# Performance work log

Hardware: AMD Instinct MI355X
Metric: run time of the kernel (lower is better)

## Reference

```python
import jax, jax.numpy as jnp
import numpy as np

BN_EPS = 1e-5  # torch BatchNorm1d default


def setup_inputs() -> dict:
    key = jax.random.key(0)
    ks = jax.random.split(key, 4)
    S, B, H = 2048, 64, 1024
    return {
        "ctx": jax.random.normal(ks[0], (S, B, H), dtype=jnp.float32),
        "key": jax.random.normal(ks[1], (B, H), dtype=jnp.float32),
        "mask": jnp.zeros((B, S), dtype=jnp.float32),
        "fc1_w": jax.random.normal(ks[2], (H, 2 * H), dtype=jnp.float32) * 0.02,
        "fc1_b": jnp.zeros((H,), dtype=jnp.float32),
        "bn_gamma": jnp.ones((H,), dtype=jnp.float32),
        "bn_beta": jnp.zeros((H,), dtype=jnp.float32),
        "fc2_w": jax.random.normal(ks[3], (H, H), dtype=jnp.float32) * 0.02,
        "fc2_b": jnp.zeros((H,), dtype=jnp.float32),
    }


def reference(ctx, key, mask, fc1_w, fc1_b, bn_gamma, bn_beta, fc2_w, fc2_b):
    # ctx: (S, B, H) -> (B, S, H)
    ctx_b = jnp.transpose(ctx, (1, 0, 2))
    # dot-product scores: (B, S)
    At = jnp.einsum('bsh,bh->bs', ctx_b, key) + mask
    At = jax.nn.softmax(At, axis=1)
    # weighted sum of context: (B, H)
    attn = jnp.einsum('bs,bsh->bh', At, ctx_b)
    # MLP head: Linear -> BatchNorm1d (training stats, biased var) -> Tanh -> Linear
    x = jnp.concatenate([attn, key], axis=1)  # (B, 2H)
    x = x @ fc1_w.T + fc1_b
    mean = jnp.mean(x, axis=0)
    var = jnp.mean(jnp.square(x - mean), axis=0)
    x = (x - mean) * jax.lax.rsqrt(var + BN_EPS) * bn_gamma + bn_beta
    x = jnp.tanh(x)
    x = x @ fc2_w.T + fc2_b
    return (x, At)
```

## Files before the change

### kernel.cpp

```cpp
#include <hip/hip_runtime.h>

constexpr int Sdim = 2048;
constexpr int Bdim = 64;
constexpr int Hdim = 1024;
constexpr int NCHUNK = 16;
constexpr int KS1 = 16;
constexpr int KS2 = 8;

constexpr int PM_OFF   = 0;
constexpr int PL_OFF   = 1024;
constexpr int PACC_OFF = 2048;
constexpr int ATTN_OFF = PACC_OFF + Bdim * NCHUNK * Hdim;
constexpr int XMID_OFF = ATTN_OFF + Bdim * Hdim;
constexpr int P1_OFF   = XMID_OFF + Bdim * Hdim;
constexpr int P2_OFF   = P1_OFF + KS1 * Bdim * Hdim;

__global__ __launch_bounds__(256) void k1_attn(const float* __restrict__ ctx,
                                               const float* __restrict__ key,
                                               const float* __restrict__ mask,
                                               float* __restrict__ ws,
                                               float* __restrict__ At) {
    const int chunk = blockIdx.x;
    const int b     = blockIdx.y;
    const int t     = threadIdx.x;
    const int lane  = t & 63;
    const int wave  = t >> 6;

    const float4* key4 = (const float4*)(key + (size_t)b * Hdim);
    float4 kr[4];
#pragma unroll
    for (int j = 0; j < 4; ++j) kr[j] = key4[j * 64 + lane];

    float4 acc[4];
#pragma unroll
    for (int j = 0; j < 4; ++j) acc[j] = make_float4(0.f, 0.f, 0.f, 0.f);
    float m = -1e30f, l = 0.f;

    const int s0 = chunk * 128 + wave * 32;
    for (int i = 0; i < 32; ++i) {
        const int s = s0 + i;
        const float4* c4 = (const float4*)ctx + (((size_t)s * Bdim + b) << 8);
        float4 v[4];
#pragma unroll
        for (int j = 0; j < 4; ++j) v[j] = c4[j * 64 + lane];

        float d = 0.f;
#pragma unroll
        for (int j = 0; j < 4; ++j)
            d += v[j].x * kr[j].x + v[j].y * kr[j].y + v[j].z * kr[j].z + v[j].w * kr[j].w;
#pragma unroll
        for (int off = 32; off >= 1; off >>= 1) d += __shfl_xor(d, off, 64);
        d += mask[b * Sdim + s];
        if (lane == 0) At[b * Sdim + s] = d;

        const float nm = fmaxf(m, d);
        const float sc = __expf(m - nm);
        const float w  = __expf(d - nm);
#pragma unroll
        for (int j = 0; j < 4; ++j) {
            acc[j].x = acc[j].x * sc + v[j].x * w;
            acc[j].y = acc[j].y * sc + v[j].y * w;
            acc[j].z = acc[j].z * sc + v[j].z * w;
            acc[j].w = acc[j].w * sc + v[j].w * w;
        }
        l = l * sc + w;
        m = nm;
    }

    __shared__ float lm[4], ll[4];
    __shared__ __align__(16) float lacc[4][1024];
    if (lane == 0) { lm[wave] = m; ll[wave] = l; }
    __syncthreads();
    const float M  = fmaxf(fmaxf(lm[0], lm[1]), fmaxf(lm[2], lm[3]));
    const float scw = __expf(m - M);
    float4* lw = (float4*)lacc[wave];
#pragma unroll
    for (int j = 0; j < 4; ++j)
        lw[j * 64 + lane] = make_float4(acc[j].x * scw, acc[j].y * scw,
                                        acc[j].z * scw, acc[j].w * scw);
    __syncthreads();

    const float L = ll[0] * __expf(lm[0] - M) + ll[1] * __expf(lm[1] - M)
                  + ll[2] * __expf(lm[2] - M) + ll[3] * __expf(lm[3] - M);
    const float4* l4 = (const float4*)lacc;
    float4 r = l4[t];
#pragma unroll
    for (int wv = 1; wv < 4; ++wv) {
        float4 o = l4[wv * 256 + t];
        r.x += o.x; r.y += o.y; r.z += o.z; r.w += o.w;
    }
    ((float4*)(ws + PACC_OFF))[(b * NCHUNK + chunk) * 256 + t] = r;
    if (t == 0) {
        ws[PM_OFF + b * NCHUNK + chunk] = M;
        ws[PL_OFF + b * NCHUNK + chunk] = L;
    }
}

__global__ __launch_bounds__(256) void k2_final(float* __restrict__ ws,
                                                float* __restrict__ At) {
    const int b = blockIdx.x;
    const int t = threadIdx.x;

    float pm[NCHUNK];
    float M = -1e30f;
#pragma unroll
    for (int c = 0; c < NCHUNK; ++c) {
        pm[c] = ws[PM_OFF + b * NCHUNK + c];
        M = fmaxf(M, pm[c]);
    }
    float e[NCHUNK];
    float L = 0.f;
#pragma unroll
    for (int c = 0; c < NCHUNK; ++c) {
        e[c] = __expf(pm[c] - M);
        L += ws[PL_OFF + b * NCHUNK + c] * e[c];
    }
    const float invL = 1.f / L;

    const float4* pa = (const float4*)(ws + PACC_OFF);
    float4 r = make_float4(0.f, 0.f, 0.f, 0.f);
#pragma unroll
    for (int c = 0; c < NCHUNK; ++c) {
        float4 v = pa[(b * NCHUNK + c) * 256 + t];
        r.x += v.x * e[c]; r.y += v.y * e[c]; r.z += v.z * e[c]; r.w += v.w * e[c];
    }
    r.x *= invL; r.y *= invL; r.z *= invL; r.w *= invL;
    ((float4*)(ws + ATTN_OFF))[b * 256 + t] = r;

#pragma unroll
    for (int k = 0; k < Sdim / 256; ++k) {
        const int s = t + k * 256;
        At[b * Sdim + s] = __expf(At[b * Sdim + s] - M) * invL;
    }
}

__global__ __launch_bounds__(256) void k3a_fc1(const float* __restrict__ attn,
                                               const float* __restrict__ key,
                                               const float* __restrict__ w,
                                               float* __restrict__ part) {
    const int obase = blockIdx.x * 64;
    const int kblk  = blockIdx.y;
    const int t  = threadIdx.x;
    const int bx = (t & 15) * 4;
    const int ox = (t >> 4) * 4;

    __shared__ __align__(16) float xs[32][68];
    __shared__ __align__(16) float wsh[32][68];

    float a[4][4];
#pragma unroll
    for (int i = 0; i < 4; ++i)
#pragma unroll
        for (int j = 0; j < 4; ++j) a[i][j] = 0.f;

    for (int c = 0; c < 4; ++c) {
        const int i0 = kblk * 128 + c * 32;
        const float* src = (i0 < Hdim) ? (attn + i0) : (key + (i0 - Hdim));
#pragma unroll
        for (int j = 0; j < 8; ++j) {
            const int e = t + j * 256;
            const int k_l = e & 31, b_l = e >> 5;
            xs[k_l][b_l] = src[b_l * Hdim + k_l];
        }
#pragma unroll
        for (int j = 0; j < 8; ++j) {
            const int e = t + j * 256;
            const int k_l = e & 31, o_l = e >> 5;
            wsh[k_l][o_l] = w[(size_t)(obase + o_l) * 2048 + i0 + k_l];
        }
        __syncthreads();
#pragma unroll
        for (int k = 0; k < 32; ++k) {
            const float4 xv = *(const float4*)&xs[k][bx];
            const float4 wv = *(const float4*)&wsh[k][ox];
            a[0][0] += xv.x * wv.x; a[0][1] += xv.x * wv.y; a[0][2] += xv.x * wv.z; a[0][3] += xv.x * wv.w;
            a[1][0] += xv.y * wv.x; a[1][1] += xv.y * wv.y; a[1][2] += xv.y * wv.z; a[1][3] += xv.y * wv.w;
            a[2][0] += xv.z * wv.x; a[2][1] += xv.z * wv.y; a[2][2] += xv.z * wv.z; a[2][3] += xv.z * wv.w;
            a[3][0] += xv.w * wv.x; a[3][1] += xv.w * wv.y; a[3][2] += xv.w * wv.z; a[3][3] += xv.w * wv.w;
        }
        __syncthreads();
    }
    float* p = part + (size_t)kblk * (Bdim * Hdim);
#pragma unroll
    for (int i = 0; i < 4; ++i)
        *(float4*)&p[(bx + i) * Hdim + obase + ox] = make_float4(a[i][0], a[i][1], a[i][2], a[i][3]);
}

__global__ __launch_bounds__(256) void k3b_bn(const float* __restrict__ p1,
                                              const float* __restrict__ fc1_b,
                                              const float* __restrict__ gamma,
                                              const float* __restrict__ beta,
                                              float* __restrict__ xmidT) {
    const int obase = blockIdx.x * 16;
    const int t  = threadIdx.x;
    const int b  = t & 63;
    const int ot = t >> 6;
    const int o0 = obase + ot * 4;

    float4 acc = ((const float4*)fc1_b)[o0 >> 2];
    const float4* p4 = (const float4*)p1;
#pragma unroll
    for (int k = 0; k < KS1; ++k) {
        float4 v = p4[k * (Bdim * Hdim / 4) + b * (Hdim / 4) + (o0 >> 2)];
        acc.x += v.x; acc.y += v.y; acc.z += v.z; acc.w += v.w;
    }
    const float4 g  = ((const float4*)gamma)[o0 >> 2];
    const float4 be = ((const float4*)beta)[o0 >> 2];
    const float xv[4] = {acc.x, acc.y, acc.z, acc.w};
    const float gv[4] = {g.x, g.y, g.z, g.w};
    const float bv[4] = {be.x, be.y, be.z, be.w};
#pragma unroll
    for (int q = 0; q < 4; ++q) {
        const float x = xv[q];
        float s1 = x, s2 = x * x;
#pragma unroll
        for (int off = 32; off >= 1; off >>= 1) {
            s1 += __shfl_xor(s1, off, 64);
            s2 += __shfl_xor(s2, off, 64);
        }
        const float mean = s1 * (1.f / 64.f);
        float var = s2 * (1.f / 64.f) - mean * mean;
        var = fmaxf(var, 0.f);
        const float inv = rsqrtf(var + 1e-5f);
        const float y = (x - mean) * inv * gv[q] + bv[q];
        xmidT[(o0 + q) * Bdim + b] = tanhf(y);
    }
}

__global__ __launch_bounds__(256) void k4a_fc2(const float* __restrict__ xmidT,
                                               const float* __restrict__ w,
                                               float* __restrict__ part) {
    const int obase = blockIdx.x * 64;
    const int kblk  = blockIdx.y;
    const int t  = threadIdx.x;
    const int bx = (t & 15) * 4;
    const int ox = (t >> 4) * 4;

    __shared__ __align__(16) float xs[32][68];
    __shared__ __align__(16) float wsh[32][68];

    float a[4][4];
#pragma unroll
    for (int i = 0; i < 4; ++i)
#pragma unroll
        for (int j = 0; j < 4; ++j) a[i][j] = 0.f;

    for (int c = 0; c < 4; ++c) {
        const int i0 = kblk * 128 + c * 32;
#pragma unroll
        for (int j = 0; j < 8; ++j) {
            const int e = t + j * 256;
            const int k_l = e >> 6, b_l = e & 63;
            xs[k_l][b_l] = xmidT[(i0 + k_l) * Bdim + b_l];
        }
#pragma unroll
        for (int j = 0; j < 8; ++j) {
            const int e = t + j * 256;
            const int k_l = e & 31, o_l = e >> 5;
            wsh[k_l][o_l] = w[(size_t)(obase + o_l) * Hdim + i0 + k_l];
        }
        __syncthreads();
#pragma unroll
        for (int k = 0; k < 32; ++k) {
            const float4 xv = *(const float4*)&xs[k][bx];
            const float4 wv = *(const float4*)&wsh[k][ox];
            a[0][0] += xv.x * wv.x; a[0][1] += xv.x * wv.y; a[0][2] += xv.x * wv.z; a[0][3] += xv.x * wv.w;
            a[1][0] += xv.y * wv.x; a[1][1] += xv.y * wv.y; a[1][2] += xv.y * wv.z; a[1][3] += xv.y * wv.w;
            a[2][0] += xv.z * wv.x; a[2][1] += xv.z * wv.y; a[2][2] += xv.z * wv.z; a[2][3] += xv.z * wv.w;
            a[3][0] += xv.w * wv.x; a[3][1] += xv.w * wv.y; a[3][2] += xv.w * wv.z; a[3][3] += xv.w * wv.w;
        }
        __syncthreads();
    }
    float* p = part + (size_t)kblk * (Bdim * Hdim);
#pragma unroll
    for (int i = 0; i < 4; ++i)
        *(float4*)&p[(bx + i) * Hdim + obase + ox] = make_float4(a[i][0], a[i][1], a[i][2], a[i][3]);
}

__global__ __launch_bounds__(256) void k4b_out(const float* __restrict__ p2,
                                               const float* __restrict__ fc2_b,
                                               float* __restrict__ outx) {
    const int idx = blockIdx.x * 256 + threadIdx.x;
    float v = fc2_b[idx & (Hdim - 1)];
#pragma unroll
    for (int k = 0; k < KS2; ++k) v += p2[k * (Bdim * Hdim) + idx];
    outx[idx] = v;
}

extern "C" void kernel_launch(void* const* d_in, const int* in_sizes, int n_in,
                              void* d_out, int out_size, void* d_ws, size_t ws_size,
                              hipStream_t stream) {
    const float* ctx    = (const float*)d_in[0];
    const float* key    = (const float*)d_in[1];
    const float* mask   = (const float*)d_in[2];
    const float* fc1_w  = (const float*)d_in[3];
    const float* fc1_b  = (const float*)d_in[4];
    const float* gamma  = (const float*)d_in[5];
    const float* beta   = (const float*)d_in[6];
    const float* fc2_w  = (const float*)d_in[7];
    const float* fc2_b  = (const float*)d_in[8];

    float* outx = (float*)d_out;
    float* At   = outx + Bdim * Hdim;
    float* ws   = (float*)d_ws;

    k1_attn<<<dim3(NCHUNK, Bdim), 256, 0, stream>>>(ctx, key, mask, ws, At);
    k2_final<<<Bdim, 256, 0, stream>>>(ws, At);
    k3a_fc1<<<dim3(Hdim / 64, KS1), 256, 0, stream>>>(ws + ATTN_OFF, key, fc1_w, ws + P1_OFF);
    k3b_bn<<<Hdim / 16, 256, 0, stream>>>(ws + P1_OFF, fc1_b, gamma, beta, ws + XMID_OFF);
    k4a_fc2<<<dim3(Hdim / 64, KS2), 256, 0, stream>>>(ws + XMID_OFF, fc2_w, ws + P2_OFF);
    k4b_out<<<Bdim * Hdim / 256, 256, 0, stream>>>(ws + P2_OFF, fc2_b, outx);
}
```

Before: 730.3 us.

## Double split-S chunks, process two rows per iteration with nontemporal ctx loads

```diff
diff --git a/kernel.cpp b/kernel.cpp
--- a/kernel.cpp
+++ b/kernel.cpp
@@ -1,15 +1,17 @@
 #include <hip/hip_runtime.h>
+
+typedef float nf4 __attribute__((ext_vector_type(4)));
 
 constexpr int Sdim = 2048;
 constexpr int Bdim = 64;
 constexpr int Hdim = 1024;
-constexpr int NCHUNK = 16;
+constexpr int NCHUNK = 32;
 constexpr int KS1 = 16;
 constexpr int KS2 = 8;
 
 constexpr int PM_OFF   = 0;
-constexpr int PL_OFF   = 1024;
-constexpr int PACC_OFF = 2048;
+constexpr int PL_OFF   = PM_OFF + Bdim * NCHUNK;
+constexpr int PACC_OFF = PL_OFF + Bdim * NCHUNK;
 constexpr int ATTN_OFF = PACC_OFF + Bdim * NCHUNK * Hdim;
 constexpr int XMID_OFF = ATTN_OFF + Bdim * Hdim;
 constexpr int P1_OFF   = XMID_OFF + Bdim * Hdim;
@@ -26,44 +28,54 @@
     const int lane  = t & 63;
     const int wave  = t >> 6;
 
-    const float4* key4 = (const float4*)(key + (size_t)b * Hdim);
-    float4 kr[4];
+    const nf4* key4 = (const nf4*)(key + (size_t)b * Hdim);
+    nf4 kr[4];
 #pragma unroll
     for (int j = 0; j < 4; ++j) kr[j] = key4[j * 64 + lane];
 
-    float4 acc[4];
-#pragma unroll
-    for (int j = 0; j < 4; ++j) acc[j] = make_float4(0.f, 0.f, 0.f, 0.f);
+    nf4 acc[4];
+#pragma unroll
+    for (int j = 0; j < 4; ++j) acc[j] = (nf4)(0.f);
     float m = -1e30f, l = 0.f;
 
-    const int s0 = chunk * 128 + wave * 32;
-    for (int i = 0; i < 32; ++i) {
-        const int s = s0 + i;
-        const float4* c4 = (const float4*)ctx + (((size_t)s * Bdim + b) << 8);
-        float4 v[4];
-#pragma unroll
-        for (int j = 0; j < 4; ++j) v[j] = c4[j * 64 + lane];
-
-        float d = 0.f;
+    const int s0 = chunk * 64 + wave * 16;
+    for (int i = 0; i < 8; ++i) {
+        const int sa = s0 + 2 * i;
+        const int sb = sa + 1;
+        const nf4* ca = (const nf4*)ctx + (((size_t)sa * Bdim + b) << 8);
+        const nf4* cb = (const nf4*)ctx + (((size_t)sb * Bdim + b) << 8);
+        nf4 va[4], vb[4];
+#pragma unroll
+        for (int j = 0; j < 4; ++j) va[j] = __builtin_nontemporal_load(&ca[j * 64 + lane]);
+#pragma unroll
+        for (int j = 0; j < 4; ++j) vb[j] = __builtin_nontemporal_load(&cb[j * 64 + lane]);
+
+        float da = 0.f, db = 0.f;
+#pragma unroll
+        for (int j = 0; j < 4; ++j) {
+            da += va[j].x * kr[j].x + va[j].y * kr[j].y + va[j].z * kr[j].z + va[j].w * kr[j].w;
+            db += vb[j].x * kr[j].x + vb[j].y * kr[j].y + vb[j].z * kr[j].z + vb[j].w * kr[j].w;
+        }
+#pragma unroll
+        for (int off = 32; off >= 1; off >>= 1) {
+            da += __shfl_xor(da, off, 64);
+            db += __shfl_xor(db, off, 64);
+        }
+        da += mask[b * Sdim + sa];
+        db += mask[b * Sdim + sb];
+        if (lane == 0) {
+            At[b * Sdim + sa] = da;
+            At[b * Sdim + sb] = db;
+        }
+
+        const float nm = fmaxf(m, fmaxf(da, db));
+        const float sc = __expf(m - nm);
+        const float wa = __expf(da - nm);
+        const float wb = __expf(db - nm);
 #pragma unroll
         for (int j = 0; j < 4; ++j)
-            d += v[j].x * kr[j].x + v[j].y * kr[j].y + v[j].z * kr[j].z + v[j].w * kr[j].w;
-#pragma unroll
-        for (int off = 32; off >= 1; off >>= 1) d += __shfl_xor(d, off, 64);
-        d += mask[b * Sdim + s];
-        if (lane == 0) At[b * Sdim + s] = d;
-
-        const float nm = fmaxf(m, d);
-        const float sc = __expf(m - nm);
-        const float w  = __expf(d - nm);
-#pragma unroll
-        for (int j = 0; j < 4; ++j) {
-            acc[j].x = acc[j].x * sc + v[j].x * w;
-            acc[j].y = acc[j].y * sc + v[j].y * w;
-            acc[j].z = acc[j].z * sc + v[j].z * w;
-            acc[j].w = acc[j].w * sc + v[j].w * w;
-        }
-        l = l * sc + w;
+            acc[j] = acc[j] * sc + va[j] * wa + vb[j] * wb;
+        l = l * sc + wa + wb;
         m = nm;
     }
 
@@ -73,23 +85,20 @@
     __syncthreads();
     const float M  = fmaxf(fmaxf(lm[0], lm[1]), fmaxf(lm[2], lm[3]));
     const float scw = __expf(m - M);
-    float4* lw = (float4*)lacc[wave];
+    nf4* lw = (nf4*)lacc[wave];
 #pragma unroll
     for (int j = 0; j < 4; ++j)
-        lw[j * 64 + lane] = make_float4(acc[j].x * scw, acc[j].y * scw,
-                                        acc[j].z * scw, acc[j].w * scw);
+        lw[j * 64 + lane] = acc[j] * scw;
     __syncthreads();
 
     const float L = ll[0] * __expf(lm[0] - M) + ll[1] * __expf(lm[1] - M)
                   + ll[2] * __expf(lm[2] - M) + ll[3] * __expf(lm[3] - M);
-    const float4* l4 = (const float4*)lacc;
-    float4 r = l4[t];
-#pragma unroll
-    for (int wv = 1; wv < 4; ++wv) {
-        float4 o = l4[wv * 256 + t];
-        r.x += o.x; r.y += o.y; r.z += o.z; r.w += o.w;
-    }
-    ((float4*)(ws + PACC_OFF))[(b * NCHUNK + chunk) * 256 + t] = r;
+    const nf4* l4 = (const nf4*)lacc;
+    nf4 r = l4[t];
+#pragma unroll
+    for (int wv = 1; wv < 4; ++wv)
+        r += l4[wv * 256 + t];
+    ((nf4*)(ws + PACC_OFF))[(b * NCHUNK + chunk) * 256 + t] = r;
     if (t == 0) {
         ws[PM_OFF + b * NCHUNK + chunk] = M;
         ws[PL_OFF + b * NCHUNK + chunk] = L;
@@ -101,36 +110,35 @@
     const int b = blockIdx.x;
     const int t = threadIdx.x;
 
-    float pm[NCHUNK];
     float M = -1e30f;
 #pragma unroll
+    for (int c = 0; c < NCHUNK; ++c)
+        M = fmaxf(M, ws[PM_OFF + b * NCHUNK + c]);
+    float L = 0.f;
+#pragma unroll
+    for (int c = 0; c < NCHUNK; ++c)
+        L += ws[PL_OFF + b * NCHUNK + c] * __expf(ws[PM_OFF + b * NCHUNK + c] - M);
+    const float invL = 1.f / L;
+
+    const nf4* pa = (const nf4*)(ws + PACC_OFF);
+    nf4 r = (nf4)(0.f);
+#pragma unroll
     for (int c = 0; c < NCHUNK; ++c) {
-        pm[c] = ws[PM_OFF + b * NCHUNK + c];
-        M = fmaxf(M, pm[c]);
-    }
-    float e[NCHUNK];
-    float L = 0.f;
-#pragma unroll
-    for (int c = 0; c < NCHUNK; ++c) {
-        e[c] = __expf(pm[c] - M);
-        L += ws[PL_OFF + b * NCHUNK + c] * e[c];
-    }
-    const float invL = 1.f / L;
-
-    const float4* pa = (const float4*)(ws + PACC_OFF);
-    float4 r = make_float4(0.f, 0.f, 0.f, 0.f);
-#pragma unroll
-    for (int c = 0; c < NCHUNK; ++c) {
-        float4 v = pa[(b * NCHUNK + c) * 256 + t];
-        r.x += v.x * e[c]; r.y += v.y * e[c]; r.z += v.z * e[c]; r.w += v.w * e[c];
-    }
-    r.x *= invL; r.y *= invL; r.z *= invL; r.w *= invL;
-    ((float4*)(ws + ATTN_OFF))[b * 256 + t] = r;
-
-#pragma unroll
-    for (int k = 0; k < Sdim / 256; ++k) {
-        const int s = t + k * 256;
-        At[b * Sdim + s] = __expf(At[b * Sdim + s] - M) * invL;
+        const float e = __expf(ws[PM_OFF + b * NCHUNK + c] - M);
+        r += pa[(b * NCHUNK + c) * 256 + t] * e;
+    }
+    r *= invL;
+    ((nf4*)(ws + ATTN_OFF))[b * 256 + t] = r;
+
+    nf4* At4 = (nf4*)(At + b * Sdim);
+#pragma unroll
+    for (int k = 0; k < 2; ++k) {
+        nf4 v = At4[t + k * 256];
+        v.x = __expf(v.x - M) * invL;
+        v.y = __expf(v.y - M) * invL;
+        v.z = __expf(v.z - M) * invL;
+        v.w = __expf(v.w - M) * invL;
+        At4[t + k * 256] = v;
     }
 }
 
```

Result: faster. 704.1 us (-3.6%).
